# Performance work log

Hardware: AMD Instinct MI355X
Metric: run time of the kernel (lower is better)

Reference implementation:

```python
import jax, jax.numpy as jnp
import numpy as np

EMBED_DIM = 768
NUM_HEADS = 12
HEAD_DIM = EMBED_DIM // NUM_HEADS


def setup_inputs() -> dict:
    key = jax.random.key(0)
    k_x, k_wqkv, k_bqkv, k_wo, k_bo = jax.random.split(key, 5)
    B, S = 2, 4096
    x = jax.random.normal(k_x, (B, S, EMBED_DIM), dtype=jnp.float32)
    # nn.Linear default init: U(-1/sqrt(fan_in), 1/sqrt(fan_in))
    bound = 1.0 / np.sqrt(EMBED_DIM)
    w_qkv = jax.random.uniform(k_wqkv, (EMBED_DIM, 3 * EMBED_DIM), jnp.float32, -bound, bound)
    b_qkv = jax.random.uniform(k_bqkv, (3 * EMBED_DIM,), jnp.float32, -bound, bound)
    w_out = jax.random.uniform(k_wo, (EMBED_DIM, EMBED_DIM), jnp.float32, -bound, bound)
    b_out = jax.random.uniform(k_bo, (EMBED_DIM,), jnp.float32, -bound, bound)
    return {"x": x, "w_qkv": w_qkv, "b_qkv": b_qkv, "w_out": w_out, "b_out": b_out}


def reference(x, w_qkv, b_qkv, w_out, b_out):
    B, S, E = x.shape
    H, D = NUM_HEADS, HEAD_DIM
    qkv = x @ w_qkv + b_qkv                       # [B,S,3E]
    qkv = qkv.reshape(B, S, 3, H, D)
    q = qkv[:, :, 0].transpose(0, 2, 1, 3)        # [B,H,S,D]
    k = qkv[:, :, 1].transpose(0, 2, 1, 3)
    v = qkv[:, :, 2].transpose(0, 2, 1, 3)
    scores = jnp.einsum('bhqd,bhkd->bhqk', q, k) / jnp.sqrt(jnp.float32(D))
    causal = jnp.tril(jnp.ones((S, S), dtype=bool))
    scores = jnp.where(causal, scores, -jnp.inf)
    weights = jax.nn.softmax(scores, axis=-1)
    attended = jnp.einsum('bhqk,bhkd->bhqd', weights, v)  # [B,H,S,D]
    attended = attended.transpose(0, 2, 1, 3).reshape(B, S, E)
    return attended @ w_out + b_out
```

## Files before the change

kernel.cpp:

```cpp
#include <hip/hip_runtime.h>

#define EMBED 768
#define NH 12
#define HD 64
#define SEQ 4096
#define BATCH 2
#define MROWS (BATCH * SEQ)
#define N3E (3 * EMBED)

typedef short bf16x8 __attribute__((ext_vector_type(8)));
typedef float fx4 __attribute__((ext_vector_type(4)));
typedef unsigned short ushort_t;
typedef unsigned short us4 __attribute__((ext_vector_type(4)));

#if __has_builtin(__builtin_amdgcn_exp2f)
#define EXP2F(x) __builtin_amdgcn_exp2f(x)
#else
#define EXP2F(x) exp2f(x)
#endif

#define QSCALE 0.18033688011112042f

__device__ inline ushort_t f2bf(float f) {
  union { float f; unsigned int u; } x; x.f = f;
  unsigned int r = x.u + 0x7fffu + ((x.u >> 16) & 1u);
  return (ushort_t)(r >> 16);
}

__global__ __launch_bounds__(256) void convert_x(const float* __restrict__ in,
                                                 ushort_t* __restrict__ out) {
  int i = (blockIdx.x * 256 + threadIdx.x) * 8;
  float4 a = *(const float4*)(in + i);
  float4 b = *(const float4*)(in + i + 4);
  bf16x8 o;
  o[0] = f2bf(a.x); o[1] = f2bf(a.y); o[2] = f2bf(a.z); o[3] = f2bf(a.w);
  o[4] = f2bf(b.x); o[5] = f2bf(b.y); o[6] = f2bf(b.z); o[7] = f2bf(b.w);
  *(bf16x8*)(out + i) = o;
}

__global__ __launch_bounds__(256) void transpose_w(const float* __restrict__ in,
                                                   ushort_t* __restrict__ out,
                                                   int K, int N) {
  __shared__ float t[64][65];
  const int bn = blockIdx.x * 64, bk = blockIdx.y * 64;
  const int c = threadIdx.x & 63, r0 = threadIdx.x >> 6;
#pragma unroll
  for (int rr = 0; rr < 16; ++rr) {
    int row = rr * 4 + r0;
    t[row][c] = in[(size_t)(bk + row) * N + bn + c];
  }
  __syncthreads();
#pragma unroll
  for (int rr = 0; rr < 16; ++rr) {
    int row = rr * 4 + r0;
    out[(size_t)(bn + row) * K + bk + c] = f2bf(t[c][row]);
  }
}

template <int N_, int K_, bool SCATTER>
__global__ __launch_bounds__(256) void gemm_mfma(
    const ushort_t* __restrict__ A, const ushort_t* __restrict__ Bt,
    const float* __restrict__ bias, float* __restrict__ outF,
    ushort_t* __restrict__ oq, ushort_t* __restrict__ ok,
    ushort_t* __restrict__ ov) {
  __shared__ __align__(16) ushort_t As[128 * 32];
  __shared__ __align__(16) ushort_t Bs[128 * 32];
  const int tid = threadIdx.x;
  const int w = tid >> 6, lane = tid & 63;
  const int quad = lane >> 4, ln = lane & 15;
  const int bm = blockIdx.y * 128, bn = blockIdx.x * 128;
  const int wm = (w >> 1) * 64, wn = (w & 1) * 64;

  const int sr = lane >> 2;
  const int sslot = lane & 3;

  fx4 acc[4][4] = {};

  for (int k0 = 0; k0 < K_; k0 += 32) {
    __syncthreads();
#pragma unroll
    for (int r = 0; r < 2; ++r) {
      const int c = w + r * 4;
      const int m = c * 16 + sr;
      const int kk = k0 + ((sslot ^ (m & 3)) << 3);
      __builtin_amdgcn_global_load_lds(
          (const __attribute__((address_space(1))) unsigned int*)
              (A + (size_t)(bm + m) * K_ + kk),
          (__attribute__((address_space(3))) unsigned int*)(As + c * 512),
          16, 0, 0);
      __builtin_amdgcn_global_load_lds(
          (const __attribute__((address_space(1))) unsigned int*)
              (Bt + (size_t)(bn + m) * K_ + kk),
          (__attribute__((address_space(3))) unsigned int*)(Bs + c * 512),
          16, 0, 0);
    }
    __syncthreads();

    bf16x8 af[4], bfr[4];
#pragma unroll
    for (int i = 0; i < 4; ++i) {
      const int m = wm + i * 16 + ln;
      af[i] = *(const bf16x8*)(As + m * 32 + ((quad ^ (m & 3)) << 3));
    }
#pragma unroll
    for (int j = 0; j < 4; ++j) {
      const int n = wn + j * 16 + ln;
      bfr[j] = *(const bf16x8*)(Bs + n * 32 + ((quad ^ (n & 3)) << 3));
    }
#pragma unroll
    for (int i = 0; i < 4; ++i)
#pragma unroll
      for (int j = 0; j < 4; ++j)
        acc[i][j] = __builtin_amdgcn_mfma_f32_16x16x32_bf16(af[i], bfr[j],
                                                            acc[i][j], 0, 0, 0);
  }

  if (!SCATTER) {
#pragma unroll
    for (int j = 0; j < 4; ++j) {
      const int n = bn + wn + j * 16 + ln;
      const float bv = bias[n];
#pragma unroll
      for (int i = 0; i < 4; ++i) {
        const int m0 = bm + wm + i * 16 + quad * 4;
#pragma unroll
        for (int r = 0; r < 4; ++r)
          outF[(size_t)(m0 + r) * N_ + n] = acc[i][j][r] + bv;
      }
    }
  } else {
    const int t = bn / EMBED;
#pragma unroll
    for (int j = 0; j < 4; ++j) {
      const int nn = bn + wn + j * 16 + ln;
      const int rem = nn - t * EMBED;
      const int h = rem >> 6, d = rem & 63;
      const float bv = bias[nn];
#pragma unroll
      for (int i = 0; i < 4; ++i) {
        const int m0 = bm + wm + i * 16 + quad * 4;
#pragma unroll
        for (int r = 0; r < 4; ++r) {
          const int m = m0 + r;
          const int b_ = m >> 12, s = m & 4095;
          const float v = acc[i][j][r] + bv;
          if (t == 0)
            oq[((size_t)(b_ * NH + h) * SEQ + s) * HD + d] = f2bf(v * QSCALE);
          else if (t == 1)
            ok[((size_t)(b_ * NH + h) * SEQ + s) * HD + d] = f2bf(v);
          else
            ov[((size_t)(b_ * NH + h) * HD + d) * SEQ + s] = f2bf(v);
        }
      }
    }
  }
}

__global__ __launch_bounds__(256, 3) void flash_mfma(
    const ushort_t* __restrict__ qb, const ushort_t* __restrict__ kb,
    const ushort_t* __restrict__ vb, ushort_t* __restrict__ attn) {
  __shared__ __align__(16) ushort_t Ks[2][64 * 64];
  __shared__ __align__(16) ushort_t Vt[2][64 * 64];
  __shared__ __align__(16) ushort_t Ps[64][72];

  const int tid = threadIdx.x;
  const int w = tid >> 6;
  const int lane = tid & 63;
  const int quad = lane >> 4;
  const int ln = lane & 15;

  const int bh = blockIdx.x;
  const int p = blockIdx.y;
  const size_t base = (size_t)bh * SEQ * HD;
  const ushort_t* Qg = qb + base;
  const ushort_t* Kg = kb + base;
  const ushort_t* Vg = vb + base;

  const int srow = lane >> 3;
  const int sg = (lane & 7) ^ srow;

  const int b_ = bh / NH, h = bh % NH;
  const int prow = w * 16 + ln;

  for (int phase = 0; phase < 2; ++phase) {
    const int qt = (phase == 0) ? (63 - p) : p;

    bf16x8 qf0, qf1;
    {
      const ushort_t* qrow = Qg + (size_t)(qt * 64 + prow) * HD;
      qf0 = *(const bf16x8*)(qrow + quad * 8);
      qf1 = *(const bf16x8*)(qrow + 32 + quad * 8);
    }
    fx4 oacc[4] = {};
    float l_part = 0.f;

    __syncthreads();
#pragma unroll
    for (int r2 = 0; r2 < 2; ++r2) {
      const int c = w + r2 * 4;
      const int row = c * 8 + srow;
      __builtin_amdgcn_global_load_lds(
          (const __attribute__((address_space(1))) unsigned int*)
              (Kg + (size_t)row * HD + (sg << 3)),
          (__attribute__((address_space(3))) unsigned int*)(&Ks[0][c * 512]),
          16, 0, 0);
      __builtin_amdgcn_global_load_lds(
          (const __attribute__((address_space(1))) unsigned int*)
              (Vg + (size_t)row * SEQ + (sg << 3)),
          (__attribute__((address_space(3))) unsigned int*)(&Vt[0][c * 512]),
          16, 0, 0);
    }

    for (int kt = 0; kt <= qt; ++kt) {
      const int cur = kt & 1;
      __syncthreads();
      if (kt < qt) {
        const int nxt = cur ^ 1;
#pragma unroll
        for (int r2 = 0; r2 < 2; ++r2) {
          const int c = w + r2 * 4;
          const int row = c * 8 + srow;
          __builtin_amdgcn_global_load_lds(
              (const __attribute__((address_space(1))) unsigned int*)
                  (Kg + (size_t)((kt + 1) * 64 + row) * HD + (sg << 3)),
              (__attribute__((address_space(3))) unsigned int*)(&Ks[nxt][c * 512]),
              16, 0, 0);
          __builtin_amdgcn_global_load_lds(
              (const __attribute__((address_space(1))) unsigned int*)
                  (Vg + (size_t)row * SEQ + (kt + 1) * 64 + (sg << 3)),
              (__attribute__((address_space(3))) unsigned int*)(&Vt[nxt][c * 512]),
              16, 0, 0);
        }
      }

      const bool diag = (kt == qt);
      auto do_t = [&](int t) {
        uint2 pr;
        if (diag && t > w) {
          pr.x = 0u; pr.y = 0u;
        } else {
          const int R = t * 16 + ln;
          const int off = R * 64 + ((quad ^ (R & 7)) << 3);
          bf16x8 kf0 = *(const bf16x8*)(&Ks[cur][off]);
          bf16x8 kf1 = *(const bf16x8*)(&Ks[cur][off ^ 32]);
          fx4 c = {};
          c = __builtin_amdgcn_mfma_f32_16x16x32_bf16(kf0, qf0, c, 0, 0, 0);
          c = __builtin_amdgcn_mfma_f32_16x16x32_bf16(kf1, qf1, c, 0, 0, 0);
          if (diag && t == w) {
#pragma unroll
            for (int r = 0; r < 4; ++r)
              if (quad * 4 + r > ln) c[r] = -1e30f;
          }
          unsigned int u[4];
#pragma unroll
          for (int r = 0; r < 4; ++r) {
            float e = EXP2F(c[r]);
            l_part += e;
            union { float f; unsigned int u; } x; x.f = e;
            u[r] = x.u + 0x8000u;
          }
          pr.x = __builtin_amdgcn_perm(u[1], u[0], 0x07060302u);
          pr.y = __builtin_amdgcn_perm(u[3], u[2], 0x07060302u);
        }
        *(uint2*)&Ps[prow][t * 16 + quad * 4] = pr;
      };

      do_t(0);
      do_t(1);
      bf16x8 pf0 = *(const bf16x8*)&Ps[prow][quad * 8];
      do_t(2);
      do_t(3);
#pragma unroll
      for (int t = 0; t < 4; ++t) {
        const int Rv = t * 16 + ln;
        const int offv = Rv * 64 + ((quad ^ (Rv & 7)) << 3);
        bf16x8 vf = *(const bf16x8*)(&Vt[cur][offv]);
        oacc[t] = __builtin_amdgcn_mfma_f32_16x16x32_bf16(vf, pf0, oacc[t],
                                                          0, 0, 0);
      }
      bf16x8 pf1 = *(const bf16x8*)&Ps[prow][32 + quad * 8];
#pragma unroll
      for (int t = 0; t < 4; ++t) {
        const int Rv = t * 16 + ln;
        const int offv = Rv * 64 + (((4 + quad) ^ (Rv & 7)) << 3);
        bf16x8 vf = *(const bf16x8*)(&Vt[cur][offv]);
        oacc[t] = __builtin_amdgcn_mfma_f32_16x16x32_bf16(vf, pf1, oacc[t],
                                                          0, 0, 0);
      }
    }

    l_part += __shfl_xor(l_part, 16);
    l_part += __shfl_xor(l_part, 32);
    const float inv = 1.f / l_part;
    ushort_t* orow =
        attn + (size_t)(b_ * SEQ + qt * 64 + prow) * EMBED + h * HD;
#pragma unroll
    for (int t = 0; t < 4; ++t) {
      us4 o;
#pragma unroll
      for (int r = 0; r < 4; ++r) o[r] = f2bf(oacc[t][r] * inv);
      *(us4*)(orow + t * 16 + quad * 4) = o;
    }
  }
}

extern "C" void kernel_launch(void* const* d_in, const int* in_sizes, int n_in,
                              void* d_out, int out_size, void* d_ws,
                              size_t ws_size, hipStream_t stream) {
  const float* x = (const float*)d_in[0];
  const float* w_qkv = (const float*)d_in[1];
  const float* b_qkv = (const float*)d_in[2];
  const float* w_out = (const float*)d_in[3];
  const float* b_out = (const float*)d_in[4];
  float* out = (float*)d_out;

  const size_t per = (size_t)BATCH * NH * SEQ * HD;
  ushort_t* q_buf = (ushort_t*)d_ws;
  ushort_t* k_buf = q_buf + per;
  ushort_t* v_buf = k_buf + per;
  ushort_t* attn_buf = v_buf + per;
  ushort_t* xb = attn_buf + per;
  ushort_t* wqkvT = xb + per;
  ushort_t* woutT = wqkvT + (size_t)N3E * EMBED;

  convert_x<<<(MROWS * EMBED) / 2048, 256, 0, stream>>>(x, xb);
  transpose_w<<<dim3(N3E / 64, EMBED / 64), 256, 0, stream>>>(w_qkv, wqkvT,
                                                              EMBED, N3E);
  transpose_w<<<dim3(EMBED / 64, EMBED / 64), 256, 0, stream>>>(w_out, woutT,
                                                                EMBED, EMBED);

  dim3 g1(N3E / 128, MROWS / 128);
  gemm_mfma<N3E, EMBED, true><<<g1, 256, 0, stream>>>(
      xb, wqkvT, b_qkv, nullptr, q_buf, k_buf, v_buf);

  dim3 g2(BATCH * NH, 32);
  flash_mfma<<<g2, 256, 0, stream>>>(q_buf, k_buf, v_buf, attn_buf);

  dim3 g3(EMBED / 128, MROWS / 128);
  gemm_mfma<EMBED, EMBED, false><<<g3, 256, 0, stream>>>(
      attn_buf, woutT, b_out, out, nullptr, nullptr, nullptr);
}
```

Baseline: 265.7 us.

## Launch one flash block per query tile with swizzled P buffer and precomputed offsets

Replaces the paired-tile scheme, where each block handled query tiles 63-p and p, with one block per query tile over a 64-wide grid, heaviest tiles first. It also swaps the padded P staging array for an XOR-swizzled 64x64 layout, hoists the LDS offset arithmetic out of the loop, uses incrementing global pointers, and raises launch bounds to 4 blocks per SM. The aim is more parallelism and occupancy and less per-iteration address math. The cost is that the paired load balancing gives way to many unequal blocks left to the hardware scheduler.

```diff
diff --git a/kernel.cpp b/kernel.cpp
--- a/kernel.cpp
+++ b/kernel.cpp
@@ -156,12 +156,12 @@
   }
 }
 
-__global__ __launch_bounds__(256, 3) void flash_mfma(
+__global__ __launch_bounds__(256, 4) void flash_mfma(
     const ushort_t* __restrict__ qb, const ushort_t* __restrict__ kb,
     const ushort_t* __restrict__ vb, ushort_t* __restrict__ attn) {
   __shared__ __align__(16) ushort_t Ks[2][64 * 64];
   __shared__ __align__(16) ushort_t Vt[2][64 * 64];
-  __shared__ __align__(16) ushort_t Ps[64][72];
+  __shared__ __align__(16) ushort_t Ps[64 * 64];
 
   const int tid = threadIdx.x;
   const int w = tid >> 6;
@@ -170,7 +170,7 @@
   const int ln = lane & 15;
 
   const int bh = blockIdx.x;
-  const int p = blockIdx.y;
+  const int qt = 63 - (int)blockIdx.y;
   const size_t base = (size_t)bh * SEQ * HD;
   const ushort_t* Qg = qb + base;
   const ushort_t* Kg = kb + base;
@@ -178,129 +178,128 @@
 
   const int srow = lane >> 3;
   const int sg = (lane & 7) ^ srow;
+  const int row0 = w * 8 + srow;
+  const ushort_t* kp = Kg + (size_t)row0 * HD + (sg << 3);
+  const ushort_t* vp = Vg + (size_t)row0 * SEQ + (sg << 3);
+
+  const int m7 = ln & 7;
+  int koff[4], voff[2][4], pwoff[4], proff[2];
+#pragma unroll
+  for (int t = 0; t < 4; ++t) {
+    koff[t] = (t * 16 + ln) * 64 + ((quad ^ m7) << 3);
+    voff[0][t] = (t * 16 + ln) * 64 + ((quad ^ m7) << 3);
+    voff[1][t] = (t * 16 + ln) * 64 + (((4 + quad) ^ m7) << 3);
+    pwoff[t] = (w * 16 + ln) * 64 + (((t * 2 + (quad >> 1)) ^ m7) << 3) +
+               (quad & 1) * 4;
+  }
+  proff[0] = (w * 16 + ln) * 64 + ((quad ^ m7) << 3);
+  proff[1] = (w * 16 + ln) * 64 + (((4 + quad) ^ m7) << 3);
 
   const int b_ = bh / NH, h = bh % NH;
   const int prow = w * 16 + ln;
 
-  for (int phase = 0; phase < 2; ++phase) {
-    const int qt = (phase == 0) ? (63 - p) : p;
-
-    bf16x8 qf0, qf1;
-    {
-      const ushort_t* qrow = Qg + (size_t)(qt * 64 + prow) * HD;
-      qf0 = *(const bf16x8*)(qrow + quad * 8);
-      qf1 = *(const bf16x8*)(qrow + 32 + quad * 8);
-    }
-    fx4 oacc[4] = {};
-    float l_part = 0.f;
-
+  bf16x8 qf0, qf1;
+  {
+    const ushort_t* qrow = Qg + (size_t)(qt * 64 + prow) * HD;
+    qf0 = *(const bf16x8*)(qrow + quad * 8);
+    qf1 = *(const bf16x8*)(qrow + 32 + quad * 8);
+  }
+  fx4 oacc[4] = {};
+  float l_part = 0.f;
+
+#pragma unroll
+  for (int r2 = 0; r2 < 2; ++r2) {
+    __builtin_amdgcn_global_load_lds(
+        (const __attribute__((address_space(1))) unsigned int*)(kp + r2 * (32 * HD)),
+        (__attribute__((address_space(3))) unsigned int*)(&Ks[0][(w + r2 * 4) * 512]),
+        16, 0, 0);
+    __builtin_amdgcn_global_load_lds(
+        (const __attribute__((address_space(1))) unsigned int*)(vp + r2 * (32 * SEQ)),
+        (__attribute__((address_space(3))) unsigned int*)(&Vt[0][(w + r2 * 4) * 512]),
+        16, 0, 0);
+  }
+  kp += 64 * HD;
+  vp += 64;
+
+  for (int kt = 0; kt <= qt; ++kt) {
+    const int cur = kt & 1;
     __syncthreads();
-#pragma unroll
-    for (int r2 = 0; r2 < 2; ++r2) {
-      const int c = w + r2 * 4;
-      const int row = c * 8 + srow;
-      __builtin_amdgcn_global_load_lds(
-          (const __attribute__((address_space(1))) unsigned int*)
-              (Kg + (size_t)row * HD + (sg << 3)),
-          (__attribute__((address_space(3))) unsigned int*)(&Ks[0][c * 512]),
-          16, 0, 0);
-      __builtin_amdgcn_global_load_lds(
-          (const __attribute__((address_space(1))) unsigned int*)
-              (Vg + (size_t)row * SEQ + (sg << 3)),
-          (__attribute__((address_space(3))) unsigned int*)(&Vt[0][c * 512]),
-          16, 0, 0);
-    }
-
-    for (int kt = 0; kt <= qt; ++kt) {
-      const int cur = kt & 1;
-      __syncthreads();
-      if (kt < qt) {
-        const int nxt = cur ^ 1;
-#pragma unroll
-        for (int r2 = 0; r2 < 2; ++r2) {
-          const int c = w + r2 * 4;
-          const int row = c * 8 + srow;
-          __builtin_amdgcn_global_load_lds(
-              (const __attribute__((address_space(1))) unsigned int*)
-                  (Kg + (size_t)((kt + 1) * 64 + row) * HD + (sg << 3)),
-              (__attribute__((address_space(3))) unsigned int*)(&Ks[nxt][c * 512]),
-              16, 0, 0);
-          __builtin_amdgcn_global_load_lds(
-              (const __attribute__((address_space(1))) unsigned int*)
-                  (Vg + (size_t)row * SEQ + (kt + 1) * 64 + (sg << 3)),
-              (__attribute__((address_space(3))) unsigned int*)(&Vt[nxt][c * 512]),
-              16, 0, 0);
+    if (kt < qt) {
+      const int nxt = cur ^ 1;
+#pragma unroll
+      for (int r2 = 0; r2 < 2; ++r2) {
+        __builtin_amdgcn_global_load_lds(
+            (const __attribute__((address_space(1))) unsigned int*)(kp + r2 * (32 * HD)),
+            (__attribute__((address_space(3))) unsigned int*)(&Ks[nxt][(w + r2 * 4) * 512]),
+            16, 0, 0);
+        __builtin_amdgcn_global_load_lds(
+            (const __attribute__((address_space(1))) unsigned int*)(vp + r2 * (32 * SEQ)),
+            (__attribute__((address_space(3))) unsigned int*)(&Vt[nxt][(w + r2 * 4) * 512]),
+            16, 0, 0);
+      }
+      kp += 64 * HD;
+      vp += 64;
+    }
+
+    const bool diag = (kt == qt);
+    auto do_t = [&](int t) {
+      uint2 pr;
+      if (diag && t > w) {
+        pr.x = 0u; pr.y = 0u;
+      } else {
+        bf16x8 kf0 = *(const bf16x8*)(&Ks[cur][koff[t]]);
+        bf16x8 kf1 = *(const bf16x8*)(&Ks[cur][koff[t] ^ 32]);
+        fx4 c = {};
+        c = __builtin_amdgcn_mfma_f32_16x16x32_bf16(kf0, qf0, c, 0, 0, 0);
+        c = __builtin_amdgcn_mfma_f32_16x16x32_bf16(kf1, qf1, c, 0, 0, 0);
+        if (diag && t == w) {
+#pragma unroll
+          for (int r = 0; r < 4; ++r)
+            if (quad * 4 + r > ln) c[r] = -1e30f;
         }
+        unsigned int u[4];
+#pragma unroll
+        for (int r = 0; r < 4; ++r) {
+          float e = EXP2F(c[r]);
+          l_part += e;
+          union { float f; unsigned int u; } x; x.f = e;
+          u[r] = x.u + 0x8000u;
+        }
+        pr.x = __builtin_amdgcn_perm(u[1], u[0], 0x07060302u);
+        pr.y = __builtin_amdgcn_perm(u[3], u[2], 0x07060302u);
       }
-
-      const bool diag = (kt == qt);
-      auto do_t = [&](int t) {
-        uint2 pr;
-        if (diag && t > w) {
-          pr.x = 0u; pr.y = 0u;
-        } else {
-          const int R = t * 16 + ln;
-          const int off = R * 64 + ((quad ^ (R & 7)) << 3);
-          bf16x8 kf0 = *(const bf16x8*)(&Ks[cur][off]);
-          bf16x8 kf1 = *(const bf16x8*)(&Ks[cur][off ^ 32]);
-          fx4 c = {};
-          c = __builtin_amdgcn_mfma_f32_16x16x32_bf16(kf0, qf0, c, 0, 0, 0);
-          c = __builtin_amdgcn_mfma_f32_16x16x32_bf16(kf1, qf1, c, 0, 0, 0);
-          if (diag && t == w) {
-#pragma unroll
-            for (int r = 0; r < 4; ++r)
-              if (quad * 4 + r > ln) c[r] = -1e30f;
-          }
-          unsigned int u[4];
-#pragma unroll
-          for (int r = 0; r < 4; ++r) {
-            float e = EXP2F(c[r]);
-            l_part += e;
-            union { float f; unsigned int u; } x; x.f = e;
-            u[r] = x.u + 0x8000u;
-          }
-          pr.x = __builtin_amdgcn_perm(u[1], u[0], 0x07060302u);
-          pr.y = __builtin_amdgcn_perm(u[3], u[2], 0x07060302u);
-        }
-        *(uint2*)&Ps[prow][t * 16 + quad * 4] = pr;
-      };
-
-      do_t(0);
-      do_t(1);
-      bf16x8 pf0 = *(const bf16x8*)&Ps[prow][quad * 8];
-      do_t(2);
-      do_t(3);
-#pragma unroll
-      for (int t = 0; t < 4; ++t) {
-        const int Rv = t * 16 + ln;
-        const int offv = Rv * 64 + ((quad ^ (Rv & 7)) << 3);
-        bf16x8 vf = *(const bf16x8*)(&Vt[cur][offv]);
-        oacc[t] = __builtin_amdgcn_mfma_f32_16x16x32_bf16(vf, pf0, oacc[t],
-                                                          0, 0, 0);
-      }
-      bf16x8 pf1 = *(const bf16x8*)&Ps[prow][32 + quad * 8];
-#pragma unroll
-      for (int t = 0; t < 4; ++t) {
-        const int Rv = t * 16 + ln;
-        const int offv = Rv * 64 + (((4 + quad) ^ (Rv & 7)) << 3);
-        bf16x8 vf = *(const bf16x8*)(&Vt[cur][offv]);
-        oacc[t] = __builtin_amdgcn_mfma_f32_16x16x32_bf16(vf, pf1, oacc[t],
-                                                          0, 0, 0);
-      }
-    }
-
-    l_part += __shfl_xor(l_part, 16);
-    l_part += __shfl_xor(l_part, 32);
-    const float inv = 1.f / l_part;
-    ushort_t* orow =
-        attn + (size_t)(b_ * SEQ + qt * 64 + prow) * EMBED + h * HD;
+      *(uint2*)&Ps[pwoff[t]] = pr;
+    };
+
+    do_t(0);
+    do_t(1);
+    bf16x8 pf0 = *(const bf16x8*)&Ps[proff[0]];
+    do_t(2);
+    do_t(3);
 #pragma unroll
     for (int t = 0; t < 4; ++t) {
-      us4 o;
-#pragma unroll
-      for (int r = 0; r < 4; ++r) o[r] = f2bf(oacc[t][r] * inv);
-      *(us4*)(orow + t * 16 + quad * 4) = o;
-    }
+      bf16x8 vf = *(const bf16x8*)(&Vt[cur][voff[0][t]]);
+      oacc[t] = __builtin_amdgcn_mfma_f32_16x16x32_bf16(vf, pf0, oacc[t], 0, 0, 0);
+    }
+    bf16x8 pf1 = *(const bf16x8*)&Ps[proff[1]];
+#pragma unroll
+    for (int t = 0; t < 4; ++t) {
+      bf16x8 vf = *(const bf16x8*)(&Vt[cur][voff[1][t]]);
+      oacc[t] = __builtin_amdgcn_mfma_f32_16x16x32_bf16(vf, pf1, oacc[t], 0, 0, 0);
+    }
+  }
+
+  l_part += __shfl_xor(l_part, 16);
+  l_part += __shfl_xor(l_part, 32);
+  const float inv = 1.f / l_part;
+  ushort_t* orow =
+      attn + (size_t)(b_ * SEQ + qt * 64 + prow) * EMBED + h * HD;
+#pragma unroll
+  for (int t = 0; t < 4; ++t) {
+    us4 o;
+#pragma unroll
+    for (int r = 0; r < 4; ++r) o[r] = f2bf(oacc[t][r] * inv);
+    *(us4*)(orow + t * 16 + quad * 4) = o;
   }
 }
 
@@ -333,7 +332,7 @@
   gemm_mfma<N3E, EMBED, true><<<g1, 256, 0, stream>>>(
       xb, wqkvT, b_qkv, nullptr, q_buf, k_buf, v_buf);
 
-  dim3 g2(BATCH * NH, 32);
+  dim3 g2(BATCH * NH, 64);
   flash_mfma<<<g2, 256, 0, stream>>>(q_buf, k_buf, v_buf, attn_buf);
 
   dim3 g3(EMBED / 128, MROWS / 128);
```

Measured after the change: 262.2 us. Within noise of the previous version (-1.3%).
